# Optimization experiments

Hardware: AMD Instinct MI355X
Metric: run time of the kernel (lower is better)

The kernel has to match this reference:

```python
import jax, jax.numpy as jnp
import numpy as np

B, T, E, D = 64, 512, 1024, 1024  # batch, enc timesteps, enc hidden, dec hidden


def setup_inputs() -> dict:
    key = jax.random.key(0)
    ks = jax.random.split(key, 9)
    s = lambda fan_in: 1.0 / np.sqrt(fan_in)
    return {
        "hidden": jax.random.normal(ks[0], (B, D), jnp.float32),
        "decoder_out": jax.random.normal(ks[1], (B, D), jnp.float32),
        "encoder_states": jax.random.normal(ks[2], (T, B, E), jnp.float32),
        # attn: Linear(D+E -> 2E)
        "Wa": jax.random.uniform(ks[3], (2 * E, D + E), jnp.float32, -s(D + E), s(D + E)),
        "ba": jax.random.uniform(ks[4], (2 * E,), jnp.float32, -s(D + E), s(D + E)),
        # attn2: Linear(2E -> 1)
        "w2": jax.random.uniform(ks[5], (1, 2 * E), jnp.float32, -s(2 * E), s(2 * E)),
        "b2": jax.random.uniform(ks[6], (1,), jnp.float32, -s(2 * E), s(2 * E)),
        # attn_combine: Linear(D+E -> D)
        "Wc": jax.random.uniform(ks[7], (D, D + E), jnp.float32, -s(D + E), s(D + E)),
        "bc": jax.random.uniform(ks[8], (D,), jnp.float32, -s(D + E), s(D + E)),
    }


def reference(hidden, decoder_out, encoder_states, Wa, ba, w2, b2, Wc, bc):
    d = hidden.shape[1]
    # attn(cat(hidden, enc_t)) = hidden @ Wa[:, :D].T + enc_t @ Wa[:, D:].T + ba
    h_proj = hidden @ Wa[:, :d].T + ba                      # [B, 2E]
    e_proj = jnp.einsum('tbe,fe->tbf', encoder_states, Wa[:, d:])  # [T, B, 2E]
    act = jnp.tanh(h_proj[None, :, :] + e_proj)             # [T, B, 2E]
    scores = jnp.einsum('tbf,f->bt', act, w2[0]) + b2[0]    # [B, T]
    weights = jax.nn.softmax(scores, axis=-1)               # softmax over timesteps
    # weighted sum of encoder states: [B, E]
    applied = jnp.einsum('bt,tbe->be', weights, encoder_states)
    combined = jnp.concatenate([decoder_out, applied], axis=1)  # [B, D+E]
    out = jnp.tanh(combined @ Wc.T + bc)                    # [B, D]
    return out, applied
```

## Files before the change

kernel.cpp:

```cpp
#include <hip/hip_runtime.h>
#include <hip/hip_bf16.h>

#define BB 64
#define TT 512
#define EE 1024
#define DD 1024
#define BK 64

typedef __attribute__((ext_vector_type(8))) short s16x8;
typedef __attribute__((ext_vector_type(4))) float f32x4;

__device__ __forceinline__ float bf2f(unsigned short u) {
    unsigned int x = ((unsigned int)u) << 16;
    return __builtin_bit_cast(float, x);
}
__device__ __forceinline__ unsigned short f2bf(float f) {
    unsigned int u = __builtin_bit_cast(unsigned int, f);
    u += 0x7FFF + ((u >> 16) & 1);
    return (unsigned short)(u >> 16);
}
__device__ __forceinline__ float tanh_fast(float x) {
    x = fminf(fmaxf(x, -15.f), 15.f);
    float e = __expf(2.f * x);
    return (e - 1.f) / (e + 1.f);
}

__global__ __launch_bounds__(256) void conv_enc_kernel(
    const float4* __restrict__ src, ushort4* __restrict__ dst)
{
    int idx = blockIdx.x * 256 + threadIdx.x;
    float4 v = src[idx];
    ushort4 o;
    o.x = f2bf(v.x); o.y = f2bf(v.y); o.z = f2bf(v.z); o.w = f2bf(v.w);
    dst[idx] = o;
}

__global__ __launch_bounds__(256) void conv_wa_kernel(
    const float* __restrict__ Wa, unsigned short* __restrict__ WaR)
{
    int idx = blockIdx.x * 256 + threadIdx.x;
    int row = idx >> 8;
    int c4  = idx & 255;
    float4 v = *(const float4*)(Wa + (size_t)row * 2048 + 1024 + c4 * 4);
    ushort4 o;
    o.x = f2bf(v.x); o.y = f2bf(v.y); o.z = f2bf(v.z); o.w = f2bf(v.w);
    *(ushort4*)(WaR + (size_t)row * 1024 + c4 * 4) = o;
}

__global__ __launch_bounds__(256) void hproj_kernel(
    const float* __restrict__ hidden,
    const float* __restrict__ Wa,
    const float* __restrict__ ba,
    float* __restrict__ hp)
{
    __shared__ float sW[8 * 1024];
    const int tid  = threadIdx.x;
    const int lane = tid & 63;
    const int wave = tid >> 6;
    const int f0   = blockIdx.x * 8;

#pragma unroll
    for (int i = 0; i < 8; ++i) {
        int idx = i * 256 + tid;
        int fi  = idx >> 8;
        int c4  = idx & 255;
        ((float4*)sW)[idx] = *(const float4*)(Wa + (size_t)(f0 + fi) * 2048 + c4 * 4);
    }
    __syncthreads();

    for (int bi = 0; bi < 16; ++bi) {
        int b = wave * 16 + bi;
        float h[16];
#pragma unroll
        for (int j = 0; j < 16; ++j) h[j] = hidden[b * 1024 + lane + 64 * j];
#pragma unroll
        for (int fi = 0; fi < 8; ++fi) {
            float s = 0.f;
#pragma unroll
            for (int j = 0; j < 16; ++j) s += h[j] * sW[fi * 1024 + lane + 64 * j];
#pragma unroll
            for (int m = 32; m; m >>= 1) s += __shfl_xor(s, m);
            if (lane == 0) hp[(f0 + fi) * 64 + b] = s + ba[f0 + fi];
        }
    }
}

__global__ __launch_bounds__(256) void gemm_scores(
    const unsigned short* __restrict__ encB,
    const unsigned short* __restrict__ WaR,
    const float* __restrict__ hp,
    const float* __restrict__ w2,
    float* __restrict__ scores)
{
    __shared__ short sA[128 * BK];
    __shared__ short sB[128 * BK];
    __shared__ float rowAcc[128];

    const int tid  = threadIdx.x;
    const int bm   = blockIdx.x;
    const int bn   = blockIdx.y;
    const int lane = tid & 63;
    const int wave = tid >> 6;
    const int wm   = wave >> 1;
    const int wn   = wave & 1;
    const int c    = lane & 15;
    const int quad = lane >> 4;

    f32x4 acc[4][4];
#pragma unroll
    for (int mi = 0; mi < 4; ++mi)
#pragma unroll
        for (int ni = 0; ni < 4; ++ni)
#pragma unroll
            for (int r = 0; r < 4; ++r) acc[mi][ni][r] = 0.f;

    for (int k0 = 0; k0 < 1024; k0 += BK) {
#pragma unroll
        for (int i = 0; i < 4; ++i) {
            int s   = i * 256 + tid;
            int p   = s >> 7;
            int g   = (s >> 4) & 7;
            int rr  = s & 15;
            int row = p * 16 + rr;
            const unsigned short* ga = encB + (size_t)(bm * 128 + row) * 1024 + k0 + g * 8;
            __builtin_amdgcn_global_load_lds(
                (const __attribute__((address_space(1))) void*)ga,
                (__attribute__((address_space(3))) void*)&sA[s * 8], 16, 0, 0);
            const unsigned short* gb = WaR + (size_t)(bn * 128 + row) * 1024 + k0 + g * 8;
            __builtin_amdgcn_global_load_lds(
                (const __attribute__((address_space(1))) void*)gb,
                (__attribute__((address_space(3))) void*)&sB[s * 8], 16, 0, 0);
        }
        __builtin_amdgcn_s_waitcnt(0);
        __syncthreads();

#pragma unroll
        for (int kk = 0; kk < 2; ++kk) {
            s16x8 aF[4], bF[4];
#pragma unroll
            for (int mi = 0; mi < 4; ++mi)
                aF[mi] = *(const s16x8*)&sA[((wm * 4 + mi) * 128 + kk * 64 + lane) * 8];
#pragma unroll
            for (int ni = 0; ni < 4; ++ni)
                bF[ni] = *(const s16x8*)&sB[((wn * 4 + ni) * 128 + kk * 64 + lane) * 8];

#pragma unroll
            for (int mi = 0; mi < 4; ++mi)
#pragma unroll
                for (int ni = 0; ni < 4; ++ni)
                    acc[mi][ni] = __builtin_amdgcn_mfma_f32_16x16x32_bf16(
                        aF[mi], bF[ni], acc[mi][ni], 0, 0, 0);
        }
        __syncthreads();
    }

    float w2v[4];
#pragma unroll
    for (int ni = 0; ni < 4; ++ni) w2v[ni] = w2[bn * 128 + wn * 64 + ni * 16 + c];

    if (tid < 128) rowAcc[tid] = 0.f;
    __syncthreads();

#pragma unroll
    for (int mi = 0; mi < 4; ++mi) {
        int lrow0 = wm * 64 + mi * 16 + quad * 4;
        int b0    = (bm * 128 + lrow0) & 63;
        f32x4 hp4[4];
#pragma unroll
        for (int ni = 0; ni < 4; ++ni)
            hp4[ni] = *(const f32x4*)&hp[(bn * 128 + wn * 64 + ni * 16 + c) * 64 + b0];
#pragma unroll
        for (int r = 0; r < 4; ++r) {
            float s = 0.f;
#pragma unroll
            for (int ni = 0; ni < 4; ++ni)
                s += tanh_fast(acc[mi][ni][r] + hp4[ni][r]) * w2v[ni];
            s += __shfl_xor(s, 1);
            s += __shfl_xor(s, 2);
            s += __shfl_xor(s, 4);
            s += __shfl_xor(s, 8);
            if (c == 0) atomicAdd(&rowAcc[lrow0 + r], s);
        }
    }
    __syncthreads();
    if (tid < 128) {
        int grow = bm * 128 + tid;
        int b = grow & 63;
        int t = grow >> 6;
        atomicAdd(&scores[b * TT + t], rowAcc[tid]);
    }
}

__global__ __launch_bounds__(256) void softmax_kernel(float* __restrict__ scores)
{
    __shared__ float wmax[4];
    __shared__ float wsum[4];
    const int b   = blockIdx.x;
    const int tid = threadIdx.x;
    float* row = scores + b * TT;

    float v0 = row[tid], v1 = row[tid + 256];
    float m = fmaxf(v0, v1);
#pragma unroll
    for (int s = 32; s; s >>= 1) m = fmaxf(m, __shfl_xor(m, s));
    if ((tid & 63) == 0) wmax[tid >> 6] = m;
    __syncthreads();
    m = fmaxf(fmaxf(wmax[0], wmax[1]), fmaxf(wmax[2], wmax[3]));

    float e0 = __expf(v0 - m), e1 = __expf(v1 - m);
    float s = e0 + e1;
#pragma unroll
    for (int t = 32; t; t >>= 1) s += __shfl_xor(s, t);
    if ((tid & 63) == 0) wsum[tid >> 6] = s;
    __syncthreads();
    float inv = 1.f / (wsum[0] + wsum[1] + wsum[2] + wsum[3]);
    row[tid]       = e0 * inv;
    row[tid + 256] = e1 * inv;
}

__global__ __launch_bounds__(256) void applied_part_kernel(
    const unsigned short* __restrict__ encB,
    const float* __restrict__ w,
    float* __restrict__ part)
{
    __shared__ float red[128 * 8];
    const int tc  = blockIdx.x;
    const int b   = blockIdx.y;
    const int tid = threadIdx.x;
    const int eo  = tid & 127;
    const int th  = tid >> 7;
    const int e0  = eo * 8;

    float a[8];
#pragma unroll
    for (int j = 0; j < 8; ++j) a[j] = 0.f;

    for (int it = 0; it < 16; ++it) {
        int t = tc * 32 + th * 16 + it;
        float wt = w[b * TT + t];
        s16x8 v = *(const s16x8*)(encB + ((size_t)(t * BB + b)) * EE + e0);
#pragma unroll
        for (int j = 0; j < 8; ++j) a[j] += wt * bf2f((unsigned short)v[j]);
    }
    if (th == 1) {
#pragma unroll
        for (int j = 0; j < 8; ++j) red[eo * 8 + j] = a[j];
    }
    __syncthreads();
    if (th == 0) {
        float* dst = part + ((size_t)tc * 64 + b) * 1024 + e0;
#pragma unroll
        for (int j = 0; j < 8; ++j) dst[j] = a[j] + red[eo * 8 + j];
    }
}

__global__ __launch_bounds__(256) void applied_reduce_kernel(
    const float* __restrict__ part, float* __restrict__ out_applied)
{
    int idx = blockIdx.x * 256 + threadIdx.x;
    float s = 0.f;
#pragma unroll
    for (int tc = 0; tc < 16; ++tc) s += part[tc * 65536 + idx];
    out_applied[idx] = s;
}

__global__ __launch_bounds__(256) void combine_kernel(
    const float* __restrict__ dec,
    const float* applied,
    const float* __restrict__ Wc,
    const float* __restrict__ bc,
    float* out0)
{
    const int g    = blockIdx.x * 4 + (threadIdx.x >> 6);
    const int lane = threadIdx.x & 63;
    const int d    = g >> 6;
    const int b    = g & 63;

    const float4* wc4 = (const float4*)Wc + (size_t)d * 512;
    const float4* de4 = (const float4*)dec + (size_t)b * 256;
    const float4* ap4 = (const float4*)applied + (size_t)b * 256;

    float s = 0.f;
#pragma unroll
    for (int j = 0; j < 4; ++j) {
        float4 a = de4[j * 64 + lane];
        float4 wv = wc4[j * 64 + lane];
        s += a.x * wv.x + a.y * wv.y + a.z * wv.z + a.w * wv.w;
    }
#pragma unroll
    for (int j = 0; j < 4; ++j) {
        float4 a = ap4[j * 64 + lane];
        float4 wv = wc4[256 + j * 64 + lane];
        s += a.x * wv.x + a.y * wv.y + a.z * wv.z + a.w * wv.w;
    }
#pragma unroll
    for (int m = 32; m; m >>= 1) s += __shfl_xor(s, m);
    if (lane == 0) out0[b * DD + d] = tanh_fast(s + bc[d]);
}

extern "C" void kernel_launch(void* const* d_in, const int* in_sizes, int n_in,
                              void* d_out, int out_size, void* d_ws, size_t ws_size,
                              hipStream_t stream) {
    const float* hidden = (const float*)d_in[0];
    const float* dec    = (const float*)d_in[1];
    const float* enc    = (const float*)d_in[2];
    const float* Wa     = (const float*)d_in[3];
    const float* ba     = (const float*)d_in[4];
    const float* w2     = (const float*)d_in[5];
    const float* Wc     = (const float*)d_in[7];
    const float* bc     = (const float*)d_in[8];
    float* out = (float*)d_out;

    unsigned short* encB = (unsigned short*)d_ws;
    unsigned short* WaR  = encB + (size_t)33554432;
    float* hp     = (float*)(WaR + (size_t)2097152);
    float* scores = hp + 131072;
    float* part   = scores + 32768;

    hipMemsetAsync(scores, 0, BB * TT * sizeof(float), stream);
    conv_enc_kernel<<<32768, 256, 0, stream>>>((const float4*)enc, (ushort4*)encB);
    conv_wa_kernel<<<2048, 256, 0, stream>>>(Wa, WaR);
    hproj_kernel<<<256, 256, 0, stream>>>(hidden, Wa, ba, hp);
    dim3 g2(256, 16);
    gemm_scores<<<g2, 256, 0, stream>>>(encB, WaR, hp, w2, scores);
    softmax_kernel<<<BB, 256, 0, stream>>>(scores);
    dim3 g3(16, 64);
    applied_part_kernel<<<g3, 256, 0, stream>>>(encB, scores, part);
    applied_reduce_kernel<<<256, 256, 0, stream>>>(part, out + BB * DD);
    combine_kernel<<<16384, 256, 0, stream>>>(dec, out + BB * DD, Wc, bc, out);
}
```

Baseline: 608.1 us.

## Pre-tile bf16 operands into contiguous MFMA-ordered blocks and read fp32 encoder in applied

Conversion kernels now write the encoder states and Wa slice as bf16 in tile-contiguous blocks arranged in the order the GEMM loads them into LDS. Each k-step of the GEMM is then a fully contiguous 16KB copy with simple addressing. The weighted-sum kernel reads the original fp32 encoder states instead of the bf16 copy. That improves accuracy but doubles the bytes that kernel reads.

```diff
diff --git a/kernel.cpp b/kernel.cpp
--- a/kernel.cpp
+++ b/kernel.cpp
@@ -25,26 +25,72 @@
     return (e - 1.f) / (e + 1.f);
 }
 
-__global__ __launch_bounds__(256) void conv_enc_kernel(
-    const float4* __restrict__ src, ushort4* __restrict__ dst)
-{
-    int idx = blockIdx.x * 256 + threadIdx.x;
-    float4 v = src[idx];
-    ushort4 o;
-    o.x = f2bf(v.x); o.y = f2bf(v.y); o.z = f2bf(v.z); o.w = f2bf(v.w);
-    dst[idx] = o;
-}
-
-__global__ __launch_bounds__(256) void conv_wa_kernel(
-    const float* __restrict__ Wa, unsigned short* __restrict__ WaR)
-{
-    int idx = blockIdx.x * 256 + threadIdx.x;
-    int row = idx >> 8;
-    int c4  = idx & 255;
-    float4 v = *(const float4*)(Wa + (size_t)row * 2048 + 1024 + c4 * 4);
-    ushort4 o;
-    o.x = f2bf(v.x); o.y = f2bf(v.y); o.z = f2bf(v.z); o.w = f2bf(v.w);
-    *(ushort4*)(WaR + (size_t)row * 1024 + c4 * 4) = o;
+__device__ __forceinline__ int tile_slot(int row, int g) {
+    return (row >> 4) * 128 + (g >> 2) * 64 + (g & 3) * 16 + (row & 15);
+}
+
+__global__ __launch_bounds__(256) void conv_encS_kernel(
+    const float* __restrict__ enc, unsigned short* __restrict__ encS)
+{
+    __shared__ short tileL[1024 * 8];
+    const int tm  = blockIdx.x;
+    const int tk  = blockIdx.y;
+    const int tid = threadIdx.x;
+
+#pragma unroll
+    for (int it = 0; it < 4; ++it) {
+        int cidx = it * 256 + tid;
+        int row  = cidx >> 3;
+        int g    = cidx & 7;
+        const float* src = enc + (size_t)(tm * 128 + row) * 1024 + tk * 64 + g * 8;
+        float4 v0 = ((const float4*)src)[0];
+        float4 v1 = ((const float4*)src)[1];
+        short c[8];
+        c[0] = (short)f2bf(v0.x); c[1] = (short)f2bf(v0.y);
+        c[2] = (short)f2bf(v0.z); c[3] = (short)f2bf(v0.w);
+        c[4] = (short)f2bf(v1.x); c[5] = (short)f2bf(v1.y);
+        c[6] = (short)f2bf(v1.z); c[7] = (short)f2bf(v1.w);
+        *(s16x8*)&tileL[tile_slot(row, g) * 8] = *(s16x8*)c;
+    }
+    __syncthreads();
+    unsigned short* dst = encS + ((size_t)tm * 16 + tk) * 8192;
+#pragma unroll
+    for (int it = 0; it < 4; ++it) {
+        int s = it * 256 + tid;
+        *(s16x8*)&dst[s * 8] = *(const s16x8*)&tileL[s * 8];
+    }
+}
+
+__global__ __launch_bounds__(256) void conv_waS_kernel(
+    const float* __restrict__ Wa, unsigned short* __restrict__ WaS)
+{
+    __shared__ short tileL[1024 * 8];
+    const int tn  = blockIdx.x;
+    const int tk  = blockIdx.y;
+    const int tid = threadIdx.x;
+
+#pragma unroll
+    for (int it = 0; it < 4; ++it) {
+        int cidx = it * 256 + tid;
+        int row  = cidx >> 3;
+        int g    = cidx & 7;
+        const float* src = Wa + (size_t)(tn * 128 + row) * 2048 + 1024 + tk * 64 + g * 8;
+        float4 v0 = ((const float4*)src)[0];
+        float4 v1 = ((const float4*)src)[1];
+        short c[8];
+        c[0] = (short)f2bf(v0.x); c[1] = (short)f2bf(v0.y);
+        c[2] = (short)f2bf(v0.z); c[3] = (short)f2bf(v0.w);
+        c[4] = (short)f2bf(v1.x); c[5] = (short)f2bf(v1.y);
+        c[6] = (short)f2bf(v1.z); c[7] = (short)f2bf(v1.w);
+        *(s16x8*)&tileL[tile_slot(row, g) * 8] = *(s16x8*)c;
+    }
+    __syncthreads();
+    unsigned short* dst = WaS + ((size_t)tn * 16 + tk) * 8192;
+#pragma unroll
+    for (int it = 0; it < 4; ++it) {
+        int s = it * 256 + tid;
+        *(s16x8*)&dst[s * 8] = *(const s16x8*)&tileL[s * 8];
+    }
 }
 
 __global__ __launch_bounds__(256) void hproj_kernel(
@@ -86,8 +132,8 @@
 }
 
 __global__ __launch_bounds__(256) void gemm_scores(
-    const unsigned short* __restrict__ encB,
-    const unsigned short* __restrict__ WaR,
+    const unsigned short* __restrict__ encS,
+    const unsigned short* __restrict__ WaS,
     const float* __restrict__ hp,
     const float* __restrict__ w2,
     float* __restrict__ scores)
@@ -114,21 +160,17 @@
 #pragma unroll
             for (int r = 0; r < 4; ++r) acc[mi][ni][r] = 0.f;
 
-    for (int k0 = 0; k0 < 1024; k0 += BK) {
+    for (int kt = 0; kt < 16; ++kt) {
+        const unsigned short* at = encS + ((size_t)bm * 16 + kt) * 8192;
+        const unsigned short* bt = WaS  + ((size_t)bn * 16 + kt) * 8192;
 #pragma unroll
         for (int i = 0; i < 4; ++i) {
-            int s   = i * 256 + tid;
-            int p   = s >> 7;
-            int g   = (s >> 4) & 7;
-            int rr  = s & 15;
-            int row = p * 16 + rr;
-            const unsigned short* ga = encB + (size_t)(bm * 128 + row) * 1024 + k0 + g * 8;
+            int s = i * 256 + tid;
             __builtin_amdgcn_global_load_lds(
-                (const __attribute__((address_space(1))) void*)ga,
+                (const __attribute__((address_space(1))) void*)(at + s * 8),
                 (__attribute__((address_space(3))) void*)&sA[s * 8], 16, 0, 0);
-            const unsigned short* gb = WaR + (size_t)(bn * 128 + row) * 1024 + k0 + g * 8;
             __builtin_amdgcn_global_load_lds(
-                (const __attribute__((address_space(1))) void*)gb,
+                (const __attribute__((address_space(1))) void*)(bt + s * 8),
                 (__attribute__((address_space(3))) void*)&sB[s * 8], 16, 0, 0);
         }
         __builtin_amdgcn_s_waitcnt(0);
@@ -219,7 +261,7 @@
 }
 
 __global__ __launch_bounds__(256) void applied_part_kernel(
-    const unsigned short* __restrict__ encB,
+    const float* __restrict__ enc,
     const float* __restrict__ w,
     float* __restrict__ part)
 {
@@ -238,9 +280,11 @@
     for (int it = 0; it < 16; ++it) {
         int t = tc * 32 + th * 16 + it;
         float wt = w[b * TT + t];
-        s16x8 v = *(const s16x8*)(encB + ((size_t)(t * BB + b)) * EE + e0);
-#pragma unroll
-        for (int j = 0; j < 8; ++j) a[j] += wt * bf2f((unsigned short)v[j]);
+        const float* src = enc + ((size_t)(t * BB + b)) * EE + e0;
+        float4 v0 = ((const float4*)src)[0];
+        float4 v1 = ((const float4*)src)[1];
+        a[0] += wt * v0.x; a[1] += wt * v0.y; a[2] += wt * v0.z; a[3] += wt * v0.w;
+        a[4] += wt * v1.x; a[5] += wt * v1.y; a[6] += wt * v1.z; a[7] += wt * v1.w;
     }
     if (th == 1) {
 #pragma unroll
@@ -311,21 +355,23 @@
     const float* bc     = (const float*)d_in[8];
     float* out = (float*)d_out;
 
-    unsigned short* encB = (unsigned short*)d_ws;
-    unsigned short* WaR  = encB + (size_t)33554432;
-    float* hp     = (float*)(WaR + (size_t)2097152);
+    unsigned short* encS = (unsigned short*)d_ws;
+    unsigned short* WaS  = encS + (size_t)33554432;
+    float* hp     = (float*)(WaS + (size_t)2097152);
     float* scores = hp + 131072;
     float* part   = scores + 32768;
 
     hipMemsetAsync(scores, 0, BB * TT * sizeof(float), stream);
-    conv_enc_kernel<<<32768, 256, 0, stream>>>((const float4*)enc, (ushort4*)encB);
-    conv_wa_kernel<<<2048, 256, 0, stream>>>(Wa, WaR);
+    dim3 gc(256, 16);
+    conv_encS_kernel<<<gc, 256, 0, stream>>>(enc, encS);
+    dim3 gw(16, 16);
+    conv_waS_kernel<<<gw, 256, 0, stream>>>(Wa, WaS);
     hproj_kernel<<<256, 256, 0, stream>>>(hidden, Wa, ba, hp);
     dim3 g2(256, 16);
-    gemm_scores<<<g2, 256, 0, stream>>>(encB, WaR, hp, w2, scores);
+    gemm_scores<<<g2, 256, 0, stream>>>(encS, WaS, hp, w2, scores);
     softmax_kernel<<<BB, 256, 0, stream>>>(scores);
     dim3 g3(16, 64);
-    applied_part_kernel<<<g3, 256, 0, stream>>>(encB, scores, part);
+    applied_part_kernel<<<g3, 256, 0, stream>>>(enc, scores, part);
     applied_reduce_kernel<<<256, 256, 0, stream>>>(part, out + BB * DD);
     combine_kernel<<<16384, 256, 0, stream>>>(dec, out + BB * DD, Wc, bc, out);
 }
```

Measured after the change: 546.6 us. 10.1% less time.
